# Performance work log

Measured on AMD Instinct MI355X. Metric: run time of the kernel, lower is better.

Reference implementation:

```python
import jax, jax.numpy as jnp
import numpy as np

N, SEQ_LEN, HORIZON, F_IN, EMBED, HIDDEN, LAYERS = 4096, 168, 24, 32, 32, 64, 2
G4 = 4 * HIDDEN
# NOTE: original torch code calls nn.LSTM per-step WITHOUT carrying hidden state,
# so each step's LSTM starts from (h0=0, c0=0): W_hh contributes nothing, only b_hh.

def setup_inputs() -> dict:
    key = jax.random.key(0)
    ks = jax.random.split(key, 12)
    s = 0.1
    return {
        "X": jax.random.normal(ks[0], (N, SEQ_LEN, F_IN), jnp.float32),
        "y": jax.random.normal(ks[1], (N, SEQ_LEN), jnp.float32),
        "Xf": jax.random.normal(ks[2], (N, HORIZON, F_IN), jnp.float32),
        "W_embed": jax.random.normal(ks[3], (EMBED, 1), jnp.float32) * s,
        "b_embed": jax.random.normal(ks[4], (EMBED,), jnp.float32) * s,
        "W_ih": jax.random.normal(ks[5], (LAYERS, G4, EMBED + F_IN), jnp.float32) * s,  # layer1 in-dim == HIDDEN == EMBED+F_IN
        "b_ih": jax.random.normal(ks[6], (LAYERS, G4), jnp.float32) * s,
        "b_hh": jax.random.normal(ks[7], (LAYERS, G4), jnp.float32) * s,
        "W_mu": jax.random.normal(ks[8], (1, HIDDEN), jnp.float32) * s,
        "b_mu": jax.random.normal(ks[9], (1,), jnp.float32) * s,
        "W_sigma": jax.random.normal(ks[10], (1, HIDDEN), jnp.float32) * s,
        "b_sigma": jax.random.normal(ks[11], (1,), jnp.float32) * s,
    }


def reference(X, y, Xf, W_embed, b_embed, W_ih, b_ih, b_hh, W_mu, b_mu, W_sigma, b_sigma):
    num_ts = X.shape[0]
    T = SEQ_LEN + HORIZON
    Xall = jnp.concatenate([X, Xf], axis=1)  # (N, T, F_IN)
    y_pad = jnp.concatenate([y, jnp.zeros((num_ts, HORIZON), y.dtype)], axis=1)  # (N, T)
    use_y = jnp.arange(T) < SEQ_LEN  # teacher-forced region

    def step(carry, inputs):
        x_s, y_s, use = inputs  # (N, F_IN), (N,), scalar bool
        ynext = jnp.where(use, y_s[:, None], carry)  # (N, 1)
        yembed = ynext @ W_embed.T + b_embed  # (N, EMBED)
        h = jnp.concatenate([x_s, yembed], axis=1)  # (N, F_IN+EMBED)
        for l in range(LAYERS):  # single LSTM step from zero state per layer
            gates = h @ W_ih[l].T + b_ih[l] + b_hh[l]  # (N, 4H); torch gate order i,f,g,o
            i_g, f_g, g_g, o_g = jnp.split(gates, 4, axis=1)
            c = jax.nn.sigmoid(i_g) * jnp.tanh(g_g)  # f * c0 term vanishes (c0 = 0)
            h = jax.nn.sigmoid(o_g) * jnp.tanh(c)
        h = jax.nn.relu(h)
        mu = h @ W_mu.T + b_mu  # (N, 1)
        sigma = jax.nn.softplus(h @ W_sigma.T + b_sigma) + 1e-6  # log(1+exp(.)) + eps
        lik = (2.0 * np.pi * sigma ** 2) ** (-0.5) * jnp.exp(-((ynext - mu) ** 2) / (2.0 * sigma ** 2))
        return lik, (lik[:, 0], mu[:, 0], sigma[:, 0])

    carry0 = jnp.zeros((num_ts, 1), X.dtype)
    xs = (jnp.swapaxes(Xall, 0, 1), y_pad.T, use_y)
    _, (lik_t, mu_t, sigma_t) = jax.lax.scan(step, carry0, xs)  # each (T, N)
    ypred = lik_t.T[:, SEQ_LEN - 1: SEQ_LEN + HORIZON - 1]  # (N, HORIZON)
    return ypred, mu_t.T, sigma_t.T
```

## Files before the change

### kernel.cpp

```cpp
#include <hip/hip_runtime.h>
#include <math.h>

#define N_TS 4096
#define SEQ  168
#define HOR  24
#define T_ALL 192
#define F_INP 32
#define HID  64
#define NROW 192
#define NB_B (N_TS / 16)
#define L2E  1.44269504089f

typedef _Float16 half8  __attribute__((ext_vector_type(8)));
typedef _Float16 half4  __attribute__((ext_vector_type(4)));
typedef float    floatx4 __attribute__((ext_vector_type(4)));

__device__ __forceinline__ float fexp(float x)  { return __expf(x); }
__device__ __forceinline__ float ex2(float x)   { return __builtin_amdgcn_exp2f(x); }
__device__ __forceinline__ float frcp(float x)  { return __builtin_amdgcn_rcpf(x); }
__device__ __forceinline__ float softplus_(float x) { return (x > 15.0f) ? x : __logf(1.0f + fexp(x)); }

__device__ __forceinline__ float lstm_h(float ip, float gp, float op) {
    const float Ei = ex2(ip);
    const float Eg = ex2(gp);
    const float cc = (1.0f - Eg) * frcp((1.0f + Ei) * (1.0f + Eg));
    const float Ec = ex2(cc * (-2.0f * L2E));
    const float Eo = ex2(op);
    return (1.0f - Ec) * frcp((1.0f + Ec) * (1.0f + Eo));
}

__device__ __forceinline__ half8 cvt8(const float4 a, const float4 b) {
    half8 v;
    v[0]=(_Float16)a.x; v[1]=(_Float16)a.y; v[2]=(_Float16)a.z; v[3]=(_Float16)a.w;
    v[4]=(_Float16)b.x; v[5]=(_Float16)b.y; v[6]=(_Float16)b.z; v[7]=(_Float16)b.w;
    return v;
}

__global__ __launch_bounds__(256) void prep(
    const float* __restrict__ W_ih, const float* __restrict__ b_ih,
    const float* __restrict__ b_hh,
    const float* __restrict__ W_embed, const float* __restrict__ b_embed,
    _Float16* __restrict__ W16f, float* __restrict__ bsum,
    float* __restrict__ wy1, float* __restrict__ b1c)
{
    const int idx = blockIdx.x * 256 + threadIdx.x;
    for (int i = idx; i < 2 * 8 * NROW * 8; i += gridDim.x * 256) {
        const int kp  = i & 7;
        const int row = (i >> 3) % NROW;
        const int kb  = ((i >> 3) / NROW) & 7;
        const int l   = i / (8 * NROW * 8);
        const int sr  = (row < 64) ? row : row + 64;
        const float sc = (row >= 64 && row < 128) ? (-2.0f * L2E) : (-L2E);
        W16f[i] = (_Float16)(W_ih[(l * 256 + sr) * HID + kb * 8 + kp] * sc);
    }
    for (int i = idx; i < 2 * NROW; i += gridDim.x * 256) {
        const int r = i % NROW;
        const int l = i / NROW;
        const int sr = (r < 64) ? r : r + 64;
        const float sc = (r >= 64 && r < 128) ? (-2.0f * L2E) : (-L2E);
        bsum[i] = (b_ih[l * 256 + sr] + b_hh[l * 256 + sr]) * sc;
    }
    if (idx < NROW) {
        const int sr = (idx < 64) ? idx : idx + 64;
        const float sc = (idx >= 64 && idx < 128) ? (-2.0f * L2E) : (-L2E);
        const float* wrow = W_ih + sr * HID + 32;
        float s1 = 0.f, s2 = 0.f;
        #pragma unroll
        for (int k = 0; k < 32; ++k) {
            s1 = fmaf(wrow[k], W_embed[k], s1);
            s2 = fmaf(wrow[k], b_embed[k], s2);
        }
        wy1[idx] = s1 * sc;
        b1c[idx] = (b_ih[sr] + b_hh[sr] + s2) * sc;
    }
}

__global__ __launch_bounds__(256, 5) void fused(
    const float* __restrict__ X,
    const float* __restrict__ y,
    const float* __restrict__ Xf,
    const float* __restrict__ W_embed,
    const float* __restrict__ b_embed,
    const _Float16* __restrict__ W16f,
    const float* __restrict__ bsum,
    const float* __restrict__ wy1,
    const float* __restrict__ b1c,
    const float* __restrict__ W_mu,
    const float* __restrict__ b_mu,
    const float* __restrict__ W_sigma,
    const float* __restrict__ b_sigma,
    float* __restrict__ out)
{
    __shared__ union {
        struct { _Float16 Wl[12288]; _Float16 Hx[4][1024]; } A;
        struct { _Float16 slab[16 * 72]; float partm[16][4]; float parts[16][4];
                 float ylds[16]; float wyb[NROW]; float b1cb[NROW]; } B;
    } sh;

    const int tid = threadIdx.x;
    float* mu_out = out + (size_t)N_TS * HOR;
    float* sg_out = mu_out + (size_t)N_TS * T_ALL;

    if (blockIdx.x < NB_B) {
        const int w    = tid >> 6;
        const int lane = tid & 63;
        const int quad = lane >> 4;
        const int ln   = lane & 15;
        const int n0   = blockIdx.x * 16;

        if (tid < NROW) {
            sh.B.wyb[tid]  = wy1[tid];
            sh.B.b1cb[tid] = b1c[tid];
        }
        if (tid < 16)
            sh.B.ylds[tid] = y[(size_t)(n0 + tid) * SEQ + (SEQ - 1)];

        half8 B1[3];
        half8 B2[3][2];
        float bias2[3];
        #pragma unroll
        for (int j = 0; j < 3; ++j) {
            const int rt = j * 4 + w;
            B1[j] = *(const half8*)(W16f + ((size_t)quad * NROW + rt * 16 + ln) * 8);
            #pragma unroll
            for (int kt = 0; kt < 2; ++kt)
                B2[j][kt] = *(const half8*)(W16f + 12288 + ((size_t)(kt * 4 + quad) * NROW + rt * 16 + ln) * 8);
            bias2[j] = bsum[NROW + rt * 16 + ln];
        }
        const float wmu = W_mu[w * 16 + ln], wsg = W_sigma[w * 16 + ln];
        const float bmu = b_mu[0], bsg = b_sigma[0];

        const float* xfp = Xf + (size_t)(n0 + ln) * HOR * F_INP + quad * 8;
        float4 xa, xb;
        {
            const float* xp = X + ((size_t)(n0 + ln) * SEQ + (SEQ - 1)) * F_INP + quad * 8;
            xa = *(const float4*)xp;
            xb = *(const float4*)(xp + 4);
        }
        __syncthreads();

        #pragma unroll 1
        for (int st = 0; st <= HOR; ++st) {
            const half8 xf0 = cvt8(xa, xb);
            if (st < HOR) {
                xa = *(const float4*)(xfp + st * F_INP);
                xb = *(const float4*)(xfp + st * F_INP + 4);
            }

            floatx4 t0 = *(const floatx4*)(sh.B.b1cb + 0 * 64 + w * 16 + quad * 4);
            floatx4 t1 = *(const floatx4*)(sh.B.b1cb + 1 * 64 + w * 16 + quad * 4);
            floatx4 t2 = *(const floatx4*)(sh.B.b1cb + 2 * 64 + w * 16 + quad * 4);
            t0 = __builtin_amdgcn_mfma_f32_16x16x32_f16(B1[0], xf0, t0, 0, 0, 0);
            t1 = __builtin_amdgcn_mfma_f32_16x16x32_f16(B1[1], xf0, t1, 0, 0, 0);
            t2 = __builtin_amdgcn_mfma_f32_16x16x32_f16(B1[2], xf0, t2, 0, 0, 0);

            const floatx4 wy0 = *(const floatx4*)(sh.B.wyb + 0 * 64 + w * 16 + quad * 4);
            const floatx4 wy1v = *(const floatx4*)(sh.B.wyb + 1 * 64 + w * 16 + quad * 4);
            const floatx4 wy2 = *(const floatx4*)(sh.B.wyb + 2 * 64 + w * 16 + quad * 4);
            const float yn = sh.B.ylds[ln];

            half4 h1p;
            #pragma unroll
            for (int r = 0; r < 4; ++r) {
                const float ig = fmaf(yn, wy0[r], t0[r]);
                const float gg = fmaf(yn, wy1v[r], t1[r]);
                const float og = fmaf(yn, wy2[r], t2[r]);
                h1p[r] = (_Float16)lstm_h(ig, gg, og);
            }
            *(half4*)(&sh.B.slab[ln * 72 + w * 16 + quad * 4]) = h1p;
            __syncthreads();

            const half8 a0 = *(const half8*)(&sh.B.slab[ln * 72 + quad * 8]);
            const half8 a1 = *(const half8*)(&sh.B.slab[ln * 72 + 32 + quad * 8]);
            floatx4 acc[3];
            #pragma unroll
            for (int j = 0; j < 3; ++j) {
                acc[j] = (floatx4){bias2[j], bias2[j], bias2[j], bias2[j]};
                acc[j] = __builtin_amdgcn_mfma_f32_16x16x32_f16(a0, B2[j][0], acc[j], 0, 0, 0);
                acc[j] = __builtin_amdgcn_mfma_f32_16x16x32_f16(a1, B2[j][1], acc[j], 0, 0, 0);
            }

            float pmr[4], psr[4];
            #pragma unroll
            for (int r = 0; r < 4; ++r) {
                const float hh = lstm_h(acc[0][r], acc[1][r], acc[2][r]);
                const float hr = fmaxf(hh, 0.0f);
                pmr[r] = hr * wmu;
                psr[r] = hr * wsg;
            }
            #pragma unroll
            for (int off = 1; off < 16; off <<= 1) {
                #pragma unroll
                for (int r = 0; r < 4; ++r) {
                    pmr[r] += __shfl_xor(pmr[r], off, 64);
                    psr[r] += __shfl_xor(psr[r], off, 64);
                }
            }
            if (ln == 0) {
                #pragma unroll
                for (int r = 0; r < 4; ++r) {
                    sh.B.partm[quad * 4 + r][w] = pmr[r];
                    sh.B.parts[quad * 4 + r][w] = psr[r];
                }
            }
            __syncthreads();

            if (tid < 16) {
                const float4 m4 = *(const float4*)sh.B.partm[tid];
                const float4 s4 = *(const float4*)sh.B.parts[tid];
                const float mu = (m4.x + m4.y) + (m4.z + m4.w) + bmu;
                const float sg = softplus_((s4.x + s4.y) + (s4.z + s4.w) + bsg) + 1e-6f;
                const float yv = sh.B.ylds[tid];
                const float d  = yv - mu;
                const float is = frcp(sg);
                const float lik = 0.39894228040143267f * is * fexp(-0.5f * d * d * is * is);
                if (st > 0) {
                    const int nn = n0 + tid;
                    const int t  = SEQ + st - 1;
                    mu_out[(size_t)nn * T_ALL + t] = mu;
                    sg_out[(size_t)nn * T_ALL + t] = sg;
                    if (st < HOR) out[(size_t)nn * HOR + st] = lik;
                }
                sh.B.ylds[tid] = lik;
            }
            __syncthreads();
        }
        return;
    }

    const int w    = tid >> 6;
    const int lane = tid & 63;
    const int quad = lane >> 4;
    const int ln   = lane & 15;
    const int cid0 = (blockIdx.x - NB_B) * 64 + w * 16;
    const int cid  = cid0 + ln;

    half8 afr0, afr1;
    {
        const float* xp = X + (size_t)cid * F_INP + quad * 8;
        const float4 xa = *(const float4*)xp;
        const float4 xb = *(const float4*)(xp + 4);
        afr0 = cvt8(xa, xb);
        const float yv = y[cid];
        const float4 wa = *(const float4*)(W_embed + quad * 8);
        const float4 wb = *(const float4*)(W_embed + quad * 8 + 4);
        const float4 ba = *(const float4*)(b_embed + quad * 8);
        const float4 bb = *(const float4*)(b_embed + quad * 8 + 4);
        afr1[0]=(_Float16)fmaf(yv, wa.x, ba.x); afr1[1]=(_Float16)fmaf(yv, wa.y, ba.y);
        afr1[2]=(_Float16)fmaf(yv, wa.z, ba.z); afr1[3]=(_Float16)fmaf(yv, wa.w, ba.w);
        afr1[4]=(_Float16)fmaf(yv, wb.x, bb.x); afr1[5]=(_Float16)fmaf(yv, wb.y, bb.y);
        afr1[6]=(_Float16)fmaf(yv, wb.z, bb.z); afr1[7]=(_Float16)fmaf(yv, wb.w, bb.w);
    }

    #pragma unroll
    for (int c = 0; c < 6; ++c) {
        const int off = (c * 256 + tid) * 8;
        *(half8*)(sh.A.Wl + off) = *(const half8*)(W16f + off);
    }
    __syncthreads();

    _Float16* hrow = sh.A.Hx[w];
    {
        const _Float16* bp = sh.A.Wl + quad * 1536 + ln * 8;
        #pragma unroll
        for (int jt = 0; jt < 4; ++jt) {
            const float bi = bsum[jt * 16 + ln];
            const float bg = bsum[(4 + jt) * 16 + ln];
            const float bo = bsum[(8 + jt) * 16 + ln];
            floatx4 ai = (floatx4){bi, bi, bi, bi};
            floatx4 ag = (floatx4){bg, bg, bg, bg};
            floatx4 ao = (floatx4){bo, bo, bo, bo};
            ai = __builtin_amdgcn_mfma_f32_16x16x32_f16(afr0, *(const half8*)(bp + jt * 128),              ai, 0, 0, 0);
            ai = __builtin_amdgcn_mfma_f32_16x16x32_f16(afr1, *(const half8*)(bp + jt * 128 + 6144),       ai, 0, 0, 0);
            ag = __builtin_amdgcn_mfma_f32_16x16x32_f16(afr0, *(const half8*)(bp + (4 + jt) * 128),        ag, 0, 0, 0);
            ag = __builtin_amdgcn_mfma_f32_16x16x32_f16(afr1, *(const half8*)(bp + (4 + jt) * 128 + 6144), ag, 0, 0, 0);
            ao = __builtin_amdgcn_mfma_f32_16x16x32_f16(afr0, *(const half8*)(bp + (8 + jt) * 128),        ao, 0, 0, 0);
            ao = __builtin_amdgcn_mfma_f32_16x16x32_f16(afr1, *(const half8*)(bp + (8 + jt) * 128 + 6144), ao, 0, 0, 0);
            #pragma unroll
            for (int r = 0; r < 4; ++r) {
                const float hh = lstm_h(ai[r], ag[r], ao[r]);
                const int row = quad * 4 + r;
                const int col = jt * 16 + ln;
                hrow[row * 64 + (((col >> 3) ^ (row & 7)) << 3) + (col & 7)] = (_Float16)hh;
            }
        }
    }

    const half8 a0 = *(const half8*)(hrow + ln * 64 + ((quad ^ (ln & 7)) << 3));
    const half8 a1 = *(const half8*)(hrow + ln * 64 + (((4 + quad) ^ (ln & 7)) << 3));

    __syncthreads();
    #pragma unroll
    for (int c = 0; c < 6; ++c) {
        const int off = (c * 256 + tid) * 8;
        *(half8*)(sh.A.Wl + off) = *(const half8*)(W16f + 12288 + off);
    }
    __syncthreads();

    float hfin[4][4];
    {
        const _Float16* bp = sh.A.Wl + quad * 1536 + ln * 8;
        #pragma unroll
        for (int jt = 0; jt < 4; ++jt) {
            const float bi = bsum[NROW + jt * 16 + ln];
            const float bg = bsum[NROW + (4 + jt) * 16 + ln];
            const float bo = bsum[NROW + (8 + jt) * 16 + ln];
            floatx4 ai = (floatx4){bi, bi, bi, bi};
            floatx4 ag = (floatx4){bg, bg, bg, bg};
            floatx4 ao = (floatx4){bo, bo, bo, bo};
            ai = __builtin_amdgcn_mfma_f32_16x16x32_f16(a0, *(const half8*)(bp + jt * 128),              ai, 0, 0, 0);
            ai = __builtin_amdgcn_mfma_f32_16x16x32_f16(a1, *(const half8*)(bp + jt * 128 + 6144),       ai, 0, 0, 0);
            ag = __builtin_amdgcn_mfma_f32_16x16x32_f16(a0, *(const half8*)(bp + (4 + jt) * 128),        ag, 0, 0, 0);
            ag = __builtin_amdgcn_mfma_f32_16x16x32_f16(a1, *(const half8*)(bp + (4 + jt) * 128 + 6144), ag, 0, 0, 0);
            ao = __builtin_amdgcn_mfma_f32_16x16x32_f16(a0, *(const half8*)(bp + (8 + jt) * 128),        ao, 0, 0, 0);
            ao = __builtin_amdgcn_mfma_f32_16x16x32_f16(a1, *(const half8*)(bp + (8 + jt) * 128 + 6144), ao, 0, 0, 0);
            #pragma unroll
            for (int r = 0; r < 4; ++r)
                hfin[jt][r] = lstm_h(ai[r], ag[r], ao[r]);
        }
    }

    float wmu[4], wsg[4];
    #pragma unroll
    for (int jt = 0; jt < 4; ++jt) {
        wmu[jt] = W_mu[jt * 16 + ln];
        wsg[jt] = W_sigma[jt * 16 + ln];
    }
    const float bmu = b_mu[0], bsg = b_sigma[0];

    #pragma unroll
    for (int r = 0; r < 4; ++r) {
        float pm = 0.f, ps = 0.f;
        #pragma unroll
        for (int jt = 0; jt < 4; ++jt) {
            const float hr = fmaxf(hfin[jt][r], 0.0f);
            pm = fmaf(hr, wmu[jt], pm);
            ps = fmaf(hr, wsg[jt], ps);
        }
        #pragma unroll
        for (int off = 1; off < 16; off <<= 1) {
            pm += __shfl_xor(pm, off, 64);
            ps += __shfl_xor(ps, off, 64);
        }
        if (ln == 0) {
            const int cid2 = cid0 + quad * 4 + r;
            const int n = cid2 / SEQ;
            const int t = cid2 - n * SEQ;
            const float mu = pm + bmu;
            const float sg = softplus_(ps + bsg) + 1e-6f;
            mu_out[(size_t)n * T_ALL + t] = mu;
            sg_out[(size_t)n * T_ALL + t] = sg;
            if (t == SEQ - 1) {
                const float yv = y[cid2];
                const float d  = yv - mu;
                const float is = frcp(sg);
                const float lik = 0.39894228040143267f * is * fexp(-0.5f * d * d * is * is);
                out[(size_t)n * HOR] = lik;
            }
        }
    }
}

extern "C" void kernel_launch(void* const* d_in, const int* in_sizes, int n_in,
                              void* d_out, int out_size, void* d_ws, size_t ws_size,
                              hipStream_t stream) {
    const float* X       = (const float*)d_in[0];
    const float* y       = (const float*)d_in[1];
    const float* Xf      = (const float*)d_in[2];
    const float* W_embed = (const float*)d_in[3];
    const float* b_embed = (const float*)d_in[4];
    const float* W_ih    = (const float*)d_in[5];
    const float* b_ih    = (const float*)d_in[6];
    const float* b_hh    = (const float*)d_in[7];
    const float* W_mu    = (const float*)d_in[8];
    const float* b_mu    = (const float*)d_in[9];
    const float* W_sigma = (const float*)d_in[10];
    const float* b_sigma = (const float*)d_in[11];

    float* out = (float*)d_out;
    _Float16*  W16f = (_Float16*)d_ws;
    float*     bsum = (float*)((char*)d_ws + 49152);
    float*     wy1  = (float*)((char*)d_ws + 49152 + 1536);
    float*     b1c  = (float*)((char*)d_ws + 49152 + 1536 + 768);

    prep<<<96, 256, 0, stream>>>(W_ih, b_ih, b_hh, W_embed, b_embed,
                                 W16f, bsum, wy1, b1c);

    fused<<<NB_B + (N_TS * SEQ) / 64, 256, 0, stream>>>(
        X, y, Xf, W_embed, b_embed, W16f, bsum, wy1, b1c,
        W_mu, b_mu, W_sigma, b_sigma, out);
}
```

Measured before the change: 252.0 us.

## Compute likelihood redundantly per lane to drop a barrier per horizon step

The sequential horizon loop now has every thread recompute mu, sigma and the likelihood from the shared partial sums and keep the fed-back y in a register. This removes the single-thread tail section, the ylds shared buffer and one __syncthreads per step. The LDS slab drops its padding in favour of an XOR swizzle to avoid bank conflicts, and the recurrent blocks raise their wave priority with s_setprio. The trade-off is redundant transcendental work across all lanes in exchange for a shorter serial dependency chain.

After: 247.9 us. About the same (-1.6%).

```diff
diff --git a/kernel.cpp b/kernel.cpp
--- a/kernel.cpp
+++ b/kernel.cpp
@@ -91,10 +91,10 @@
     const float* __restrict__ b_sigma,
     float* __restrict__ out)
 {
-    __shared__ union {
+    __shared__ union __align__(16) {
         struct { _Float16 Wl[12288]; _Float16 Hx[4][1024]; } A;
-        struct { _Float16 slab[16 * 72]; float partm[16][4]; float parts[16][4];
-                 float ylds[16]; float wyb[NROW]; float b1cb[NROW]; } B;
+        struct { _Float16 slab[16 * 64]; float partm[16][4]; float parts[16][4];
+                 float wyb[NROW]; float b1cb[NROW]; } B;
     } sh;
 
     const int tid = threadIdx.x;
@@ -102,6 +102,7 @@
     float* sg_out = mu_out + (size_t)N_TS * T_ALL;
 
     if (blockIdx.x < NB_B) {
+        __builtin_amdgcn_s_setprio(1);
         const int w    = tid >> 6;
         const int lane = tid & 63;
         const int quad = lane >> 4;
@@ -112,8 +113,6 @@
             sh.B.wyb[tid]  = wy1[tid];
             sh.B.b1cb[tid] = b1c[tid];
         }
-        if (tid < 16)
-            sh.B.ylds[tid] = y[(size_t)(n0 + tid) * SEQ + (SEQ - 1)];
 
         half8 B1[3];
         half8 B2[3][2];
@@ -137,14 +136,35 @@
             xa = *(const float4*)xp;
             xb = *(const float4*)(xp + 4);
         }
+        float ycur = y[(size_t)(n0 + ln) * SEQ + (SEQ - 1)];
         __syncthreads();
 
         #pragma unroll 1
-        for (int st = 0; st <= HOR; ++st) {
+        for (int it = 0; it <= HOR + 1; ++it) {
+            if (it > 0) {
+                const int k = it - 1;
+                const float4 m4 = *(const float4*)sh.B.partm[ln];
+                const float4 s4 = *(const float4*)sh.B.parts[ln];
+                const float mu = (m4.x + m4.y) + (m4.z + m4.w) + bmu;
+                const float sg = softplus_((s4.x + s4.y) + (s4.z + s4.w) + bsg) + 1e-6f;
+                const float d  = ycur - mu;
+                const float is = frcp(sg);
+                const float lik = 0.39894228040143267f * is * fexp(-0.5f * d * d * is * is);
+                if (k > 0 && w == 0 && quad == 0) {
+                    const int nn = n0 + ln;
+                    const int t  = SEQ + k - 1;
+                    mu_out[(size_t)nn * T_ALL + t] = mu;
+                    sg_out[(size_t)nn * T_ALL + t] = sg;
+                    if (k < HOR) out[(size_t)nn * HOR + k] = lik;
+                }
+                ycur = lik;
+            }
+            if (it > HOR) break;
+
             const half8 xf0 = cvt8(xa, xb);
-            if (st < HOR) {
-                xa = *(const float4*)(xfp + st * F_INP);
-                xb = *(const float4*)(xfp + st * F_INP + 4);
+            if (it < HOR) {
+                xa = *(const float4*)(xfp + it * F_INP);
+                xb = *(const float4*)(xfp + it * F_INP + 4);
             }
 
             floatx4 t0 = *(const floatx4*)(sh.B.b1cb + 0 * 64 + w * 16 + quad * 4);
@@ -157,21 +177,23 @@
             const floatx4 wy0 = *(const floatx4*)(sh.B.wyb + 0 * 64 + w * 16 + quad * 4);
             const floatx4 wy1v = *(const floatx4*)(sh.B.wyb + 1 * 64 + w * 16 + quad * 4);
             const floatx4 wy2 = *(const floatx4*)(sh.B.wyb + 2 * 64 + w * 16 + quad * 4);
-            const float yn = sh.B.ylds[ln];
 
             half4 h1p;
             #pragma unroll
             for (int r = 0; r < 4; ++r) {
-                const float ig = fmaf(yn, wy0[r], t0[r]);
-                const float gg = fmaf(yn, wy1v[r], t1[r]);
-                const float og = fmaf(yn, wy2[r], t2[r]);
+                const float ig = fmaf(ycur, wy0[r], t0[r]);
+                const float gg = fmaf(ycur, wy1v[r], t1[r]);
+                const float og = fmaf(ycur, wy2[r], t2[r]);
                 h1p[r] = (_Float16)lstm_h(ig, gg, og);
             }
-            *(half4*)(&sh.B.slab[ln * 72 + w * 16 + quad * 4]) = h1p;
+            {
+                const int xblk = (2 * w + (quad >> 1)) ^ (ln & 7);
+                *(half4*)(&sh.B.slab[ln * 64 + xblk * 8 + (quad & 1) * 4]) = h1p;
+            }
             __syncthreads();
 
-            const half8 a0 = *(const half8*)(&sh.B.slab[ln * 72 + quad * 8]);
-            const half8 a1 = *(const half8*)(&sh.B.slab[ln * 72 + 32 + quad * 8]);
+            const half8 a0 = *(const half8*)(&sh.B.slab[ln * 64 + ((quad ^ (ln & 7)) << 3)]);
+            const half8 a1 = *(const half8*)(&sh.B.slab[ln * 64 + (((4 + quad) ^ (ln & 7)) << 3)]);
             floatx4 acc[3];
             #pragma unroll
             for (int j = 0; j < 3; ++j) {
@@ -202,26 +224,6 @@
                     sh.B.partm[quad * 4 + r][w] = pmr[r];
                     sh.B.parts[quad * 4 + r][w] = psr[r];
                 }
-            }
-            __syncthreads();
-
-            if (tid < 16) {
-                const float4 m4 = *(const float4*)sh.B.partm[tid];
-                const float4 s4 = *(const float4*)sh.B.parts[tid];
-                const float mu = (m4.x + m4.y) + (m4.z + m4.w) + bmu;
-                const float sg = softplus_((s4.x + s4.y) + (s4.z + s4.w) + bsg) + 1e-6f;
-                const float yv = sh.B.ylds[tid];
-                const float d  = yv - mu;
-                const float is = frcp(sg);
-                const float lik = 0.39894228040143267f * is * fexp(-0.5f * d * d * is * is);
-                if (st > 0) {
-                    const int nn = n0 + tid;
-                    const int t  = SEQ + st - 1;
-                    mu_out[(size_t)nn * T_ALL + t] = mu;
-                    sg_out[(size_t)nn * T_ALL + t] = sg;
-                    if (st < HOR) out[(size_t)nn * HOR + st] = lik;
-                }
-                sh.B.ylds[tid] = lik;
             }
             __syncthreads();
         }
```
